# Optimization experiments

Hardware: AMD Instinct MI355X
Metric: run time of the kernel (lower is better)

Reference implementation:

```python
import jax, jax.numpy as jnp
import numpy as np

B, S, DIM = 4, 2048, 2048
H, KVH, HD = 32, 8, 64
REPEATS = H // KVH
SCALE = HD ** -0.5


def _rope(x, cos, sin):
    # x: (B, S, Hn, HD); cos/sin: (S, HD//2)
    xr = x[..., 0::2]
    xi = x[..., 1::2]
    c = cos[:, None, :]  # (S, 1, HD//2) broadcasts over heads
    s = sin[:, None, :]
    out_r = xr * c - xi * s
    out_i = xr * s + xi * c
    return jnp.stack([out_r, out_i], axis=-1).reshape(x.shape)


def setup_inputs() -> dict:
    key = jax.random.key(0)
    ks = jax.random.split(key, 5)
    x = jax.random.normal(ks[0], (B, S, DIM), dtype=jnp.float32)
    wq = jax.random.normal(ks[1], (H * HD, DIM), dtype=jnp.float32) * 0.02
    wk = jax.random.normal(ks[2], (KVH * HD, DIM), dtype=jnp.float32) * 0.02
    wv = jax.random.normal(ks[3], (KVH * HD, DIM), dtype=jnp.float32) * 0.02
    wo = jax.random.normal(ks[4], (DIM, H * HD), dtype=jnp.float32) * 0.02
    # standard RoPE frequencies: freqs_cis = exp(i * t * theta)
    inv_freq = 1.0 / (10000.0 ** (jnp.arange(0, HD, 2, dtype=jnp.float32) / HD))
    angles = jnp.arange(S, dtype=jnp.float32)[:, None] * inv_freq[None, :]  # (S, HD//2)
    return {
        "x": x, "wq": wq, "wk": wk, "wv": wv, "wo": wo,
        "freqs_cos": jnp.cos(angles), "freqs_sin": jnp.sin(angles),
    }


def reference(x, wq, wk, wv, wo, freqs_cos, freqs_sin):
    b, s, _ = x.shape
    q = (x @ wq.T).reshape(b, s, H, HD)
    k = (x @ wk.T).reshape(b, s, KVH, HD)
    v = (x @ wv.T).reshape(b, s, KVH, HD)
    q = _rope(q, freqs_cos, freqs_sin)
    k = _rope(k, freqs_cos, freqs_sin)
    k_rep = jnp.repeat(k, REPEATS, axis=2)  # (B,S,H,HD)
    v_rep = jnp.repeat(v, REPEATS, axis=2)
    # NOTE: faithful to source - q is NOT transposed to (B,H,S,HD), so the
    # matmul contracts head_dim at each token, producing (B,S,H,H) scores
    # (mixing across heads per position), softmaxed over the last head axis.
    scores = jnp.einsum('bshd,bsed->bshe', q, k_rep) * SCALE  # (B,S,H,H)
    weights = jax.nn.softmax(scores, axis=-1)
    out = jnp.einsum('bshe,bsed->bshd', weights, v_rep)  # (B,S,H,HD)
    out = out.reshape(b, s, H * HD)
    return out @ wo.T
```

## Files before the change

kernel.cpp:

```cpp
#include <hip/hip_runtime.h>

typedef unsigned short u16;
typedef __bf16 bf16x8 __attribute__((ext_vector_type(8)));
typedef float f32x4 __attribute__((ext_vector_type(4)));

#define AS1 __attribute__((address_space(1)))
#define AS3 __attribute__((address_space(3)))

__device__ inline u16 f2bf(float f) {
    union { float f; unsigned u; } c; c.f = f;
    unsigned u = c.u;
    u += 0x7fffu + ((u >> 16) & 1u);
    return (u16)(u >> 16);
}
__device__ inline float bf2f(u16 b) {
    union { unsigned u; float f; } c; c.u = ((unsigned)b) << 16;
    return c.f;
}

__device__ inline void async_cp16(const void* g, void* l) {
    __builtin_amdgcn_global_load_lds((const AS1 void*)g, (AS3 void*)l, 16, 0, 0);
}

__global__ __launch_bounds__(256)
void f32_to_bf16_x8(const float* __restrict__ src, u16* __restrict__ dst) {
    int i = (blockIdx.x * 256 + threadIdx.x) * 8;
    float4 f0 = *(const float4*)(src + i);
    float4 f1 = *(const float4*)(src + i + 4);
    union { u16 h[8]; uint4 v; } o;
    o.h[0] = f2bf(f0.x); o.h[1] = f2bf(f0.y);
    o.h[2] = f2bf(f0.z); o.h[3] = f2bf(f0.w);
    o.h[4] = f2bf(f1.x); o.h[5] = f2bf(f1.y);
    o.h[6] = f2bf(f1.z); o.h[7] = f2bf(f1.w);
    *(uint4*)(dst + i) = o.v;
}

__global__ __launch_bounds__(256)
void conv_weights(const float* __restrict__ wq, const float* __restrict__ wk,
                  const float* __restrict__ wv, const float* __restrict__ wo,
                  u16* __restrict__ wqkv, u16* __restrict__ wo_bf) {
    int i = (blockIdx.x * 256 + threadIdx.x) * 4;
    const float* src;
    u16* dst;
    if (i < 4194304)       { src = wq + i;           dst = wqkv + i; }
    else if (i < 5242880)  { src = wk + (i-4194304); dst = wqkv + i; }
    else if (i < 6291456)  { src = wv + (i-5242880); dst = wqkv + i; }
    else                   { src = wo + (i-6291456); dst = wo_bf + (i-6291456); }
    float4 f = *(const float4*)src;
    union { u16 h[4]; uint2 v; } o;
    o.h[0] = f2bf(f.x); o.h[1] = f2bf(f.y);
    o.h[2] = f2bf(f.z); o.h[3] = f2bf(f.w);
    *(uint2*)dst = o.v;
}

template <bool BF16_OUT>
__global__ __launch_bounds__(256)
void gemm_bt(const u16* __restrict__ A, const u16* __restrict__ B,
             void* __restrict__ Cout, int N, int K) {
    __shared__ u16 ldsA[128 * 64];
    __shared__ u16 ldsB[128 * 64];

    const int tid  = threadIdx.x;
    const int wave = tid >> 6;
    const int lane = tid & 63;
    const int row0 = blockIdx.x * 128;
    const int col0 = blockIdx.y * 128;
    const int waveM = (wave >> 1) * 64;
    const int waveN = (wave & 1) * 64;
    const int lm   = lane & 15;
    const int quad = lane >> 4;

    const int sr  = lane >> 3;
    const int stR = 8 * wave + sr;
    const int stC = ((lane & 7) ^ sr) * 8;
    const u16* gA = A + (size_t)(row0 + stR) * K + stC;
    const u16* gB = B + (size_t)(col0 + stR) * K + stC;
    char* lA = (char*)ldsA + wave * 1024;
    char* lB = (char*)ldsB + wave * 1024;
    const size_t g32K = (size_t)32 * K;

    f32x4 acc[4][4];
#pragma unroll
    for (int i = 0; i < 4; i++)
#pragma unroll
        for (int j = 0; j < 4; j++) acc[i][j] = (f32x4){0.f, 0.f, 0.f, 0.f};

    int aOff[2][4], bOff[2][4];
#pragma unroll
    for (int s = 0; s < 2; s++)
#pragma unroll
        for (int mi = 0; mi < 4; mi++) {
            int rA = waveM + mi * 16 + lm;
            int rB = waveN + mi * 16 + lm;
            int c  = (4 * s + quad) ^ (lm & 7);
            aOff[s][mi] = rA * 128 + c * 16;
            bOff[s][mi] = rB * 128 + c * 16;
        }

    for (int kb = 0; kb < K; kb += 64) {
#pragma unroll
        for (int i = 0; i < 4; i++)
            async_cp16(gA + i * g32K + kb, lA + i * 4096);
#pragma unroll
        for (int i = 0; i < 4; i++)
            async_cp16(gB + i * g32K + kb, lB + i * 4096);
        __syncthreads();

#pragma unroll
        for (int s = 0; s < 2; s++) {
            bf16x8 af[4], bg[4];
#pragma unroll
            for (int mi = 0; mi < 4; mi++)
                af[mi] = *(const bf16x8*)((const char*)ldsA + aOff[s][mi]);
#pragma unroll
            for (int ni = 0; ni < 4; ni++)
                bg[ni] = *(const bf16x8*)((const char*)ldsB + bOff[s][ni]);
#pragma unroll
            for (int mi = 0; mi < 4; mi++)
#pragma unroll
                for (int ni = 0; ni < 4; ni++)
                    acc[mi][ni] = __builtin_amdgcn_mfma_f32_16x16x32_bf16(
                        af[mi], bg[ni], acc[mi][ni], 0, 0, 0);
        }
        __syncthreads();
    }

    const int rbase = row0 + waveM + quad * 4;
    const int cbase = col0 + waveN + lm;
    if (BF16_OUT) {
        u16* C = (u16*)Cout;
#pragma unroll
        for (int mi = 0; mi < 4; mi++)
#pragma unroll
            for (int r = 0; r < 4; r++) {
                size_t ro = (size_t)(rbase + mi * 16 + r) * N;
#pragma unroll
                for (int ni = 0; ni < 4; ni++)
                    C[ro + cbase + ni * 16] = f2bf(acc[mi][ni][r]);
            }
    } else {
        float* C = (float*)Cout;
#pragma unroll
        for (int mi = 0; mi < 4; mi++)
#pragma unroll
            for (int r = 0; r < 4; r++) {
                size_t ro = (size_t)(rbase + mi * 16 + r) * N;
#pragma unroll
                for (int ni = 0; ni < 4; ni++)
                    C[ro + cbase + ni * 16] = acc[mi][ni][r];
            }
    }
}

__global__ __launch_bounds__(256)
void attn_tok(const u16* __restrict__ qkv, u16* __restrict__ out) {
    __shared__ float kvf[1024];
    const int tok = blockIdx.x;
    const int t = threadIdx.x;
    const u16* qrow = qkv + (size_t)tok * 3072;

    {
        uint2 w = *(const uint2*)(qrow + 2048 + t * 4);
        kvf[t * 4 + 0] = bf2f((u16)(w.x & 0xffff));
        kvf[t * 4 + 1] = bf2f((u16)(w.x >> 16));
        kvf[t * 4 + 2] = bf2f((u16)(w.y & 0xffff));
        kvf[t * 4 + 3] = bf2f((u16)(w.y >> 16));
    }
    __syncthreads();

    const int h = t >> 3, j = t & 7;
    float qf[8];
    {
        uint4 w = *(const uint4*)(qrow + h * 64 + j * 8);
        unsigned ws4[4] = {w.x, w.y, w.z, w.w};
#pragma unroll
        for (int i = 0; i < 4; i++) {
            qf[2 * i]     = bf2f((u16)(ws4[i] & 0xffff));
            qf[2 * i + 1] = bf2f((u16)(ws4[i] >> 16));
        }
    }

    float s[8];
#pragma unroll
    for (int g = 0; g < 8; g++) {
        const float* kk = kvf + g * 64 + j * 8;
        float a = 0.f;
#pragma unroll
        for (int d = 0; d < 8; d++) a += qf[d] * kk[d];
        s[g] = a;
    }
#pragma unroll
    for (int g = 0; g < 8; g++) {
        s[g] += __shfl_xor(s[g], 1);
        s[g] += __shfl_xor(s[g], 2);
        s[g] += __shfl_xor(s[g], 4);
    }
    float m = -1e30f;
#pragma unroll
    for (int g = 0; g < 8; g++) { s[g] *= 0.125f; m = fmaxf(m, s[g]); }
    float p[8], l = 0.f;
#pragma unroll
    for (int g = 0; g < 8; g++) { p[g] = __expf(s[g] - m); l += p[g]; }
    float rl = 1.f / l;

    float o[8] = {0, 0, 0, 0, 0, 0, 0, 0};
#pragma unroll
    for (int g = 0; g < 8; g++) {
        float w = p[g] * rl;
        const float* vv = kvf + 512 + g * 64 + j * 8;
#pragma unroll
        for (int d = 0; d < 8; d++) o[d] += w * vv[d];
    }

    unsigned po[4];
#pragma unroll
    for (int i = 0; i < 4; i++)
        po[i] = (unsigned)f2bf(o[2 * i]) | ((unsigned)f2bf(o[2 * i + 1]) << 16);
    uint4 wo_; wo_.x = po[0]; wo_.y = po[1]; wo_.z = po[2]; wo_.w = po[3];
    *(uint4*)(out + (size_t)tok * 2048 + h * 64 + j * 8) = wo_;
}

extern "C" void kernel_launch(void* const* d_in, const int* in_sizes, int n_in,
                              void* d_out, int out_size, void* d_ws, size_t ws_size,
                              hipStream_t stream) {
    const float* x  = (const float*)d_in[0];
    const float* wq = (const float*)d_in[1];
    const float* wk = (const float*)d_in[2];
    const float* wv = (const float*)d_in[3];
    const float* wo = (const float*)d_in[4];

    u16* x_bf  = (u16*)d_ws;
    u16* wqkv  = x_bf  + 16777216;
    u16* wo_bf = wqkv  + 6291456;
    u16* qkv   = wo_bf + 4194304;
    u16* attn  = qkv   + 25165824;

    dim3 blk(256);
    f32_to_bf16_x8<<<8192, blk, 0, stream>>>(x, x_bf);
    conv_weights<<<10240, blk, 0, stream>>>(wq, wk, wv, wo, wqkv, wo_bf);

    gemm_bt<true><<<dim3(64, 24), blk, 0, stream>>>(x_bf, wqkv, qkv, 3072, 2048);

    attn_tok<<<8192, blk, 0, stream>>>(qkv, attn);

    gemm_bt<false><<<dim3(64, 16), blk, 0, stream>>>(attn, wo_bf, (float*)d_out,
                                                     2048, 2048);
}
```

Baseline: 375.1 us.

## Prefetch next GEMM K-tile into registers while computing current tile

Replaces the direct global-to-LDS async copies in the bf16 GEMM with register-staged loads. The loads for the next K block are issued before the MFMA work on the current block and written to LDS after a barrier. This aims to hide global memory latency behind compute. In exchange it adds register pressure and a second barrier per iteration, and the single LDS buffer still serializes the store with compute.

```diff
diff --git a/kernel.cpp b/kernel.cpp
--- a/kernel.cpp
+++ b/kernel.cpp
@@ -3,9 +3,6 @@
 typedef unsigned short u16;
 typedef __bf16 bf16x8 __attribute__((ext_vector_type(8)));
 typedef float f32x4 __attribute__((ext_vector_type(4)));
-
-#define AS1 __attribute__((address_space(1)))
-#define AS3 __attribute__((address_space(3)))
 
 __device__ inline u16 f2bf(float f) {
     union { float f; unsigned u; } c; c.f = f;
@@ -16,10 +13,6 @@
 __device__ inline float bf2f(u16 b) {
     union { unsigned u; float f; } c; c.u = ((unsigned)b) << 16;
     return c.f;
-}
-
-__device__ inline void async_cp16(const void* g, void* l) {
-    __builtin_amdgcn_global_load_lds((const AS1 void*)g, (AS3 void*)l, 16, 0, 0);
 }
 
 __global__ __launch_bounds__(256)
@@ -70,13 +63,14 @@
     const int lm   = lane & 15;
     const int quad = lane >> 4;
 
-    const int sr  = lane >> 3;
-    const int stR = 8 * wave + sr;
-    const int stC = ((lane & 7) ^ sr) * 8;
-    const u16* gA = A + (size_t)(row0 + stR) * K + stC;
-    const u16* gB = B + (size_t)(col0 + stR) * K + stC;
-    char* lA = (char*)ldsA + wave * 1024;
-    char* lB = (char*)ldsB + wave * 1024;
+    const int sr  = (tid >> 3) & 7;
+    const int stR = (tid >> 6) * 8 + ((tid >> 3) & 7);
+    const int srow = 8 * wave + (lane >> 3);
+    const int gcol = (((lane & 7) ^ (lane >> 3)) * 8);
+    const u16* pA = A + (size_t)(row0 + srow) * K + gcol;
+    const u16* pB = B + (size_t)(col0 + srow) * K + gcol;
+    u16* wA = ldsA + srow * 64 + (lane & 7) * 8;
+    u16* wB = ldsB + srow * 64 + (lane & 7) * 8;
     const size_t g32K = (size_t)32 * K;
 
     f32x4 acc[4][4];
@@ -97,14 +91,26 @@
             bOff[s][mi] = rB * 128 + c * 16;
         }
 
-    for (int kb = 0; kb < K; kb += 64) {
-#pragma unroll
-        for (int i = 0; i < 4; i++)
-            async_cp16(gA + i * g32K + kb, lA + i * 4096);
-#pragma unroll
-        for (int i = 0; i < 4; i++)
-            async_cp16(gB + i * g32K + kb, lB + i * 4096);
-        __syncthreads();
+    uint4 ra[4], rb[4];
+#pragma unroll
+    for (int i = 0; i < 4; i++) ra[i] = *(const uint4*)(pA + i * g32K);
+#pragma unroll
+    for (int i = 0; i < 4; i++) rb[i] = *(const uint4*)(pB + i * g32K);
+#pragma unroll
+    for (int i = 0; i < 4; i++) *(uint4*)(wA + i * 2048) = ra[i];
+#pragma unroll
+    for (int i = 0; i < 4; i++) *(uint4*)(wB + i * 2048) = rb[i];
+    __syncthreads();
+
+    for (int kb = 0;;) {
+        const int nkb = kb + 64;
+        const bool more = nkb < K;
+        if (more) {
+#pragma unroll
+            for (int i = 0; i < 4; i++) ra[i] = *(const uint4*)(pA + nkb + i * g32K);
+#pragma unroll
+            for (int i = 0; i < 4; i++) rb[i] = *(const uint4*)(pB + nkb + i * g32K);
+        }
 
 #pragma unroll
         for (int s = 0; s < 2; s++) {
@@ -122,7 +128,15 @@
                     acc[mi][ni] = __builtin_amdgcn_mfma_f32_16x16x32_bf16(
                         af[mi], bg[ni], acc[mi][ni], 0, 0, 0);
         }
+        if (!more) break;
+
         __syncthreads();
+#pragma unroll
+        for (int i = 0; i < 4; i++) *(uint4*)(wA + i * 2048) = ra[i];
+#pragma unroll
+        for (int i = 0; i < 4; i++) *(uint4*)(wB + i * 2048) = rb[i];
+        __syncthreads();
+        kb = nkb;
     }
 
     const int rbase = row0 + waveM + quad * 4;
```

Result: slower. 879.1 us (+134.4%).

## Double-buffer LDS tiles in GEMM to overlap global loads with MFMA

Applied to the files above, without the earlier changes.

The GEMM kernel now holds two LDS buffers for the A and B tiles. It issues the async global-to-LDS copy for the next K block before computing on the current one, and drops to one barrier per iteration. The aim is to hide global load latency behind matrix-core work. In exchange, LDS use doubles to 64KB per block, which may lower occupancy.

```diff
diff --git a/kernel.cpp b/kernel.cpp
--- a/kernel.cpp
+++ b/kernel.cpp
@@ -57,8 +57,8 @@
 __global__ __launch_bounds__(256)
 void gemm_bt(const u16* __restrict__ A, const u16* __restrict__ B,
              void* __restrict__ Cout, int N, int K) {
-    __shared__ u16 ldsA[128 * 64];
-    __shared__ u16 ldsB[128 * 64];
+    __shared__ u16 ldsA[2][128 * 64];
+    __shared__ u16 ldsB[2][128 * 64];
 
     const int tid  = threadIdx.x;
     const int wave = tid >> 6;
@@ -70,13 +70,12 @@
     const int lm   = lane & 15;
     const int quad = lane >> 4;
 
-    const int sr  = lane >> 3;
-    const int stR = 8 * wave + sr;
-    const int stC = ((lane & 7) ^ sr) * 8;
-    const u16* gA = A + (size_t)(row0 + stR) * K + stC;
-    const u16* gB = B + (size_t)(col0 + stR) * K + stC;
-    char* lA = (char*)ldsA + wave * 1024;
-    char* lB = (char*)ldsB + wave * 1024;
+    const int srow = 8 * wave + (lane >> 3);
+    const int gcol = (((lane & 7) ^ (lane >> 3)) * 8);
+    const u16* pA = A + (size_t)(row0 + srow) * K + gcol;
+    const u16* pB = B + (size_t)(col0 + srow) * K + gcol;
+    char* const lAbase = (char*)ldsA + wave * 1024;
+    char* const lBbase = (char*)ldsB + wave * 1024;
     const size_t g32K = (size_t)32 * K;
 
     f32x4 acc[4][4];
@@ -97,24 +96,35 @@
             bOff[s][mi] = rB * 128 + c * 16;
         }
 
+#pragma unroll
+    for (int i = 0; i < 4; i++) async_cp16(pA + i * g32K, lAbase + i * 4096);
+#pragma unroll
+    for (int i = 0; i < 4; i++) async_cp16(pB + i * g32K, lBbase + i * 4096);
+    __syncthreads();
+
+    int buf = 0;
     for (int kb = 0; kb < K; kb += 64) {
-#pragma unroll
-        for (int i = 0; i < 4; i++)
-            async_cp16(gA + i * g32K + kb, lA + i * 4096);
-#pragma unroll
-        for (int i = 0; i < 4; i++)
-            async_cp16(gB + i * g32K + kb, lB + i * 4096);
-        __syncthreads();
-
+        const int nkb = kb + 64;
+        if (nkb < K) {
+            char* dA = lAbase + (buf ^ 1) * 16384;
+            char* dB = lBbase + (buf ^ 1) * 16384;
+#pragma unroll
+            for (int i = 0; i < 4; i++) async_cp16(pA + nkb + i * g32K, dA + i * 4096);
+#pragma unroll
+            for (int i = 0; i < 4; i++) async_cp16(pB + nkb + i * g32K, dB + i * 4096);
+        }
+
+        const char* rA = (const char*)ldsA + buf * 16384;
+        const char* rB = (const char*)ldsB + buf * 16384;
 #pragma unroll
         for (int s = 0; s < 2; s++) {
             bf16x8 af[4], bg[4];
 #pragma unroll
             for (int mi = 0; mi < 4; mi++)
-                af[mi] = *(const bf16x8*)((const char*)ldsA + aOff[s][mi]);
+                af[mi] = *(const bf16x8*)(rA + aOff[s][mi]);
 #pragma unroll
             for (int ni = 0; ni < 4; ni++)
-                bg[ni] = *(const bf16x8*)((const char*)ldsB + bOff[s][ni]);
+                bg[ni] = *(const bf16x8*)(rB + bOff[s][ni]);
 #pragma unroll
             for (int mi = 0; mi < 4; mi++)
 #pragma unroll
@@ -122,7 +132,11 @@
                     acc[mi][ni] = __builtin_amdgcn_mfma_f32_16x16x32_bf16(
                         af[mi], bg[ni], acc[mi][ni], 0, 0, 0);
         }
-        __syncthreads();
+
+        if (nkb < K) {
+            __syncthreads();
+            buf ^= 1;
+        }
     }
 
     const int rbase = row0 + waveM + quad * 4;
```

After: 395.5 us. 5.4% more time.
